# Kernel optimization log

Measured on AMD Instinct MI355X. Metric: run time of the kernel, lower is better.

Reference implementation:

```python
import jax, jax.numpy as jnp
import numpy as np
from jax import lax

C = 128; H = 28; W = 28
VID_LENS = [32, 96, 64, 48, 80, 40, 88, 64]  # sums to 512
T_TOTAL = sum(VID_LENS)


def setup_inputs() -> dict:
    key = jax.random.key(0)
    ks = jax.random.split(key, 6)
    fan2 = C * 9
    fan1 = C * 3
    return {
        "x": jax.random.normal(ks[0], (T_TOTAL, C, H, W), dtype=jnp.float32),
        "vid_lens": jnp.array(VID_LENS, dtype=jnp.int32),
        "w_sp": jax.random.normal(ks[1], (C, C, 3, 3), dtype=jnp.float32) / np.sqrt(fan2),
        "b_sp": jax.random.normal(ks[2], (C,), dtype=jnp.float32) * 0.01,
        "w_t": jax.random.normal(ks[3], (C, C, 3), dtype=jnp.float32) / np.sqrt(fan1),
        "b_t": jax.random.normal(ks[4], (C,), dtype=jnp.float32) * 0.01,
        "alpha": jnp.full((C,), 0.25, dtype=jnp.float32),  # MultiNL ~ per-channel PReLU
    }


def _forward(x, vid_lens, w_sp, b_sp, w_t, b_t, alpha):
    projection = x
    # spatial 3x3 conv, stride 1, padding 1 (SAME), NCHW
    y = lax.conv_general_dilated(
        x, w_sp, window_strides=(1, 1), padding="SAME",
        dimension_numbers=("NCHW", "OIHW", "NCHW")) + b_sp[None, :, None, None]

    # Ragged temporal conv1d (k=3, pad=1) over concatenated time axis.
    # Zero the temporal neighbors at segment boundaries so each video is
    # convolved independently (equivalent to per-segment zero padding).
    T = y.shape[0]
    ends = jnp.cumsum(vid_lens)            # segment end indices (exclusive)
    starts = ends - vid_lens               # segment start indices
    start_mask = jnp.zeros((T,), bool).at[starts].set(True)
    end_mask = jnp.zeros((T,), bool).at[ends - 1].set(True)

    y_prev = jnp.where(start_mask[:, None, None, None], 0.0, jnp.roll(y, 1, axis=0))
    y_next = jnp.where(end_mask[:, None, None, None], 0.0, jnp.roll(y, -1, axis=0))

    # conv1d along time == per-tap channel-mixing matmul
    z = (jnp.einsum("oc,tchw->tohw", w_t[:, :, 0], y_prev)
         + jnp.einsum("oc,tchw->tohw", w_t[:, :, 1], y)
         + jnp.einsum("oc,tchw->tohw", w_t[:, :, 2], y_next)
         + b_t[None, :, None, None])

    # MultiNL modeled as per-channel PReLU
    z = jnp.where(z >= 0, z, alpha[None, :, None, None] * z)
    return z + projection


def reference(x, vid_lens, w_sp, b_sp, w_t, b_t, alpha):
    out = _forward(x, vid_lens, w_sp, b_sp, w_t, b_t, alpha)
    return (out, vid_lens)  # lengths are unchanged (k=3, pad=1)
```

## Files before the change

kernel.cpp:

```cpp
#include <hip/hip_runtime.h>

#define TT   512
#define CH   128
#define HWP  784
#define NSEG 8
#define NOUT 51380224

typedef short bf16x8  __attribute__((ext_vector_type(8)));
typedef float f32x4   __attribute__((ext_vector_type(4)));
typedef int   i32x4   __attribute__((ext_vector_type(4)));
typedef unsigned short u16x4 __attribute__((ext_vector_type(4)));

__device__ inline unsigned short f2bf(float f) {
    unsigned u = __builtin_bit_cast(unsigned, f);
    u += 0x7fffu + ((u >> 16) & 1u);
    return (unsigned short)(u >> 16);
}
__device__ inline int swz(int st) { return ((st ^ (st >> 4)) & 15) << 4; }

__device__ inline void gld_lds16(const void* g, void* l) {
    __builtin_amdgcn_global_load_lds(
        (const __attribute__((address_space(1))) void*)g,
        (__attribute__((address_space(3))) void*)l, 16, 0, 0);
}

__global__ void repack_wsp(const float* __restrict__ w, short* __restrict__ wA) {
    int s = blockIdx.x * 256 + threadIdx.x;
    if (s >= 128 * 128 * 9) return;
    int co = s / 1152, r = s % 1152, ci = r / 9, kh = (r % 9) / 3, kw = r % 3;
    int tap = kh * 3 + kw;
    int dst = tap * 16384 + (co >> 4) * 2048 + (ci >> 5) * 512 +
              ((ci >> 3) & 3) * 128 + (co & 15) * 8 + (ci & 7);
    wA[dst] = (short)f2bf(w[s]);
}

__global__ void repack_wt2(const float* __restrict__ w, short* __restrict__ wAt) {
    int s = blockIdx.x * 256 + threadIdx.x;
    if (s >= 128 * 128 * 3) return;
    int o = s / 384, r = s % 384, i = r / 3, tap = r % 3;
    int dst = tap * 16384 + (o >> 4) * 2048 + (i >> 5) * 512 +
              ((i >> 3) & 3) * 128 + (o & 15) * 8 + (i & 7);
    wAt[dst] = (short)f2bf(w[s]);
}

__global__ __launch_bounds__(512, 4) void spatial_mfma(
    const float* __restrict__ x, const short* __restrict__ wA,
    const float* __restrict__ b_sp, unsigned short* __restrict__ yT)
{
    __shared__ __align__(16) short xs[282 * 128];
    const int t = blockIdx.y, blockh = blockIdx.x * 8;
    const int tid = threadIdx.x;

    for (int it = 0; it < 9; ++it) {
        int u = it * 512 + tid;
        if (u < 4480) {
            int cp = u / 70, pg = u % 70;
            int rl = pg / 7, g = pg % 7;
            int rr = blockh - 1 + rl;
            float4 f0 = make_float4(0.f, 0.f, 0.f, 0.f), f1 = f0;
            if (rr >= 0 && rr < 28) {
                const float* p0 = &x[((size_t)(t * CH + 2 * cp)) * HWP + rr * 28 + g * 4];
                f0 = *(const float4*)p0;
                f1 = *(const float4*)(p0 + HWP);
            }
            float a0[4] = {f0.x, f0.y, f0.z, f0.w}, a1[4] = {f1.x, f1.y, f1.z, f1.w};
#pragma unroll
            for (int j = 0; j < 4; ++j) {
                int st = 1 + pg * 4 + j;
                unsigned val = (unsigned)f2bf(a0[j]) | ((unsigned)f2bf(a1[j]) << 16);
                int addr = (st << 8) + (cp << 2);
                addr ^= swz(st);
                *(unsigned*)((char*)xs + addr) = val;
            }
        }
    }
    __syncthreads();

    const int wid = tid >> 6, l = tid & 63;
    const int wm = wid & 1, rg = (wid >> 1) & 1, nfh = wid >> 2;
    const int l15 = l & 15, kgrp = l >> 4;
    const int h0 = blockh + rg * 4;
    if (h0 >= 28) return;

    int st0[4], mL[4], mR[4];
#pragma unroll
    for (int nfi = 0; nfi < 4; ++nfi) {
        int pl = (nfh * 4 + nfi) * 16 + l15;
        int plc = (pl < 112) ? pl : 0;
        st0[nfi] = plc + 29 + rg * 112;
        int w28 = plc % 28;
        mL[nfi] = (w28 != 0)  ? -1 : 0;
        mR[nfi] = (w28 != 27) ? -1 : 0;
    }

    f32x4 acc[4][4];
#pragma unroll
    for (int m = 0; m < 4; ++m)
#pragma unroll
        for (int n = 0; n < 4; ++n) acc[m][n] = (f32x4){0.f, 0.f, 0.f, 0.f};

    const bf16x8* wAv = (const bf16x8*)wA;

    for (int tap = 0; tap < 9; ++tap) {
        int kh = tap / 3, kw = tap % 3;
        int off = (kh - 1) * 28 + (kw - 1);
#pragma unroll
        for (int ks = 0; ks < 4; ++ks) {
            bf16x8 a0 = wAv[((tap * 8 + wm * 4 + 0) * 4 + ks) * 64 + l];
            bf16x8 a1 = wAv[((tap * 8 + wm * 4 + 1) * 4 + ks) * 64 + l];
            bf16x8 a2 = wAv[((tap * 8 + wm * 4 + 2) * 4 + ks) * 64 + l];
            bf16x8 a3 = wAv[((tap * 8 + wm * 4 + 3) * 4 + ks) * 64 + l];
#pragma unroll
            for (int nfi = 0; nfi < 4; ++nfi) {
                int st = st0[nfi] + off;
                int addr = (st << 8) + (ks << 6) + (kgrp << 4);
                addr ^= swz(st);
                i32x4 bi = *(const i32x4*)((const char*)xs + addr);
                int msk = (kw == 0) ? mL[nfi] : ((kw == 2) ? mR[nfi] : -1);
                bi = bi & msk;
                bf16x8 b = __builtin_bit_cast(bf16x8, bi);
                acc[0][nfi] = __builtin_amdgcn_mfma_f32_16x16x32_bf16(a0, b, acc[0][nfi], 0, 0, 0);
                acc[1][nfi] = __builtin_amdgcn_mfma_f32_16x16x32_bf16(a1, b, acc[1][nfi], 0, 0, 0);
                acc[2][nfi] = __builtin_amdgcn_mfma_f32_16x16x32_bf16(a2, b, acc[2][nfi], 0, 0, 0);
                acc[3][nfi] = __builtin_amdgcn_mfma_f32_16x16x32_bf16(a3, b, acc[3][nfi], 0, 0, 0);
            }
        }
    }

#pragma unroll
    for (int m = 0; m < 4; ++m) {
        int cob = wm * 64 + m * 16 + kgrp * 4;
        float4 bs = *(const float4*)&b_sp[cob];
        float bsa[4] = {bs.x, bs.y, bs.z, bs.w};
#pragma unroll
        for (int nfi = 0; nfi < 4; ++nfi) {
            int pl = (nfh * 4 + nfi) * 16 + l15;
            if (nfh == 1 && nfi == 3) continue;
            int px = h0 * 28 + pl;
            u16x4 pk;
#pragma unroll
            for (int r = 0; r < 4; ++r) pk[r] = f2bf(acc[m][nfi][r] + bsa[r]);
            *(u16x4*)&yT[((size_t)t * HWP + px) * CH + cob] = pk;
        }
    }
}

__global__ __launch_bounds__(256, 4) void temporal_mfma(
    const unsigned short* __restrict__ yT, const short* __restrict__ wAt,
    const float* __restrict__ b_t, const float* __restrict__ alpha,
    const float* __restrict__ x, const int* __restrict__ vid_lens,
    float* __restrict__ out)
{
    __shared__ __align__(16) char ldsT[29696];

    const int chunk = blockIdx.x, t = blockIdx.y;
    const int tid = threadIdx.x, wid = tid >> 6, l = tid & 63;
    const int l15 = l & 15, kgrp = l >> 4;
    const int sx = l15 & 7;

    bool isS = false, isE = false;
    {
        int cum = 0;
        for (int s = 0; s < NSEG; ++s) {
            if (t == cum) isS = true;
            cum += vid_lens[s];
            if (t == cum - 1) isE = true;
        }
    }
    const bool tapAct[3] = {!isS, true, !isE};

    auto stage = [&](int s) {
        int tap = s >> 1, kp = s & 1;
        if (!tapAct[tap]) return;
        int tp = t + tap - 1;
        const char* yb = (const char*)yT + (size_t)tp * HWP * 256;
        char* buf = ldsT + (s & 1) * 14336;
#pragma unroll
        for (int r = 0; r < 4; ++r) {
            int c = r * 256 + wid * 64 + l;
            if (r < 3 || wid < 2) {
                int px = c >> 3, sp = c & 7;
                int ssrc = sp ^ (px & 7);
                const char* g = yb + ((size_t)(chunk * 112 + px)) * 256 + kp * 128 + ssrc * 16;
                char* ldst = buf + (r * 256 + wid * 64) * 16;
                gld_lds16(g, ldst);
            }
        }
    };

    f32x4 acc[2][7];
#pragma unroll
    for (int m = 0; m < 2; ++m)
#pragma unroll
        for (int n = 0; n < 7; ++n) acc[m][n] = (f32x4){0.f, 0.f, 0.f, 0.f};

    const bf16x8* wAv = (const bf16x8*)wAt;

    stage(0);
    __syncthreads();

    for (int s = 0; s < 6; ++s) {
        if (s < 5) stage(s + 1);
        int tap = s >> 1, kp = s & 1;
        if (tapAct[tap]) {
            const char* buf = ldsT + (s & 1) * 14336;
            bf16x8 a[2][2];
#pragma unroll
            for (int m = 0; m < 2; ++m)
#pragma unroll
                for (int k1 = 0; k1 < 2; ++k1)
                    a[m][k1] = wAv[((tap * 8 + wid * 2 + m) * 4 + kp * 2 + k1) * 64 + l];
#pragma unroll
            for (int k1 = 0; k1 < 2; ++k1) {
#pragma unroll
                for (int nf = 0; nf < 7; ++nf) {
                    int addr = (nf * 16 + l15) * 128 + ((k1 * 4 + kgrp) ^ sx) * 16;
                    i32x4 bi = *(const i32x4*)(buf + addr);
                    bf16x8 b = __builtin_bit_cast(bf16x8, bi);
                    acc[0][nf] = __builtin_amdgcn_mfma_f32_16x16x32_bf16(a[0][k1], b, acc[0][nf], 0, 0, 0);
                    acc[1][nf] = __builtin_amdgcn_mfma_f32_16x16x32_bf16(a[1][k1], b, acc[1][nf], 0, 0, 0);
                }
            }
        }
        __syncthreads();
    }

    float* fl = (float*)ldsT;
    const int wbase = wid * 1856;
#pragma unroll
    for (int m = 0; m < 2; ++m) {
#pragma unroll
        for (int nf = 0; nf < 7; ++nf)
#pragma unroll
            for (int rr = 0; rr < 4; ++rr)
                fl[wbase + (kgrp * 4 + rr) * 116 + nf * 16 + l15] = acc[m][nf][rr];
#pragma unroll
        for (int j = 0; j < 7; ++j) {
            int idx = j * 64 + l;
            int co_r = idx / 28, q = idx % 28;
            f32x4 v4 = *(const f32x4*)&fl[wbase + co_r * 116 + q * 4];
            int co_g = wid * 32 + m * 16 + co_r;
            float bt = b_t[co_g], al = alpha[co_g];
            size_t gi = ((size_t)(t * CH + co_g)) * HWP + chunk * 112 + q * 4;
            float4 xv = *(const float4*)&x[gi];
            float xr[4] = {xv.x, xv.y, xv.z, xv.w};
            float rrv[4];
#pragma unroll
            for (int e = 0; e < 4; ++e) {
                float v = v4[e] + bt;
                v = (v >= 0.f) ? v : al * v;
                rrv[e] = v + xr[e];
            }
            *(float4*)&out[gi] = make_float4(rrv[0], rrv[1], rrv[2], rrv[3]);
        }
        __syncthreads();
    }
}

__global__ void write_lens(const int* __restrict__ vid_lens, float* __restrict__ out) {
    int i = threadIdx.x;
    if (i < NSEG) out[NOUT + i] = (float)vid_lens[i];
}

extern "C" void kernel_launch(void* const* d_in, const int* in_sizes, int n_in,
                              void* d_out, int out_size, void* d_ws, size_t ws_size,
                              hipStream_t stream) {
    const float* x        = (const float*)d_in[0];
    const int*   vid_lens = (const int*)d_in[1];
    const float* w_sp     = (const float*)d_in[2];
    const float* b_sp     = (const float*)d_in[3];
    const float* w_t      = (const float*)d_in[4];
    const float* b_t      = (const float*)d_in[5];
    const float* alpha    = (const float*)d_in[6];
    float* out = (float*)d_out;

    unsigned short* yT = (unsigned short*)d_ws;
    short* wA  = (short*)((char*)d_ws + 102760448);
    short* wAt = (short*)((char*)d_ws + 102760448 + 294912);

    repack_wsp<<<576, 256, 0, stream>>>(w_sp, wA);
    repack_wt2<<<192, 256, 0, stream>>>(w_t, wAt);
    spatial_mfma<<<dim3(4, 512), 512, 0, stream>>>(x, wA, b_sp, yT);
    temporal_mfma<<<dim3(7, 512), 256, 0, stream>>>(yT, wAt, b_t, alpha, x, vid_lens, out);
    write_lens<<<1, 64, 0, stream>>>(vid_lens, out);
}
```

Measured before the change: 332.6 us.

## Pad spatial LDS tile, remap warp tiling, and write channel-interleaved 16-byte yT stores

The spatial conv LDS tile gains zero-padded border columns (30-wide rows), so the per-tap left/right edge masks go away. Each warp's tile changes from 4 channel blocks by 4 pixel fragments to 2 channel blocks by all 7 pixel fragments, which removes the wasted padded fragment. The per-tap LDS addresses are now precomputed once per tap. The output is written as 16-byte vectors in a permuted channel order, and the temporal weight repack is permuted to match. s_setprio is also added around the MFMA loops in both kernels. Risks include extra LDS, more accumulator registers, and correctness of the channel permutation.

```diff
diff --git a/kernel.cpp b/kernel.cpp
--- a/kernel.cpp
+++ b/kernel.cpp
@@ -9,14 +9,13 @@
 typedef short bf16x8  __attribute__((ext_vector_type(8)));
 typedef float f32x4   __attribute__((ext_vector_type(4)));
 typedef int   i32x4   __attribute__((ext_vector_type(4)));
-typedef unsigned short u16x4 __attribute__((ext_vector_type(4)));
+typedef unsigned short u16x8 __attribute__((ext_vector_type(8)));
 
 __device__ inline unsigned short f2bf(float f) {
     unsigned u = __builtin_bit_cast(unsigned, f);
     u += 0x7fffu + ((u >> 16) & 1u);
     return (unsigned short)(u >> 16);
 }
-__device__ inline int swz(int st) { return ((st ^ (st >> 4)) & 15) << 4; }
 
 __device__ inline void gld_lds16(const void* g, void* l) {
     __builtin_amdgcn_global_load_lds(
@@ -37,25 +36,37 @@
 __global__ void repack_wt2(const float* __restrict__ w, short* __restrict__ wAt) {
     int s = blockIdx.x * 256 + threadIdx.x;
     if (s >= 128 * 128 * 3) return;
-    int o = s / 384, r = s % 384, i = r / 3, tap = r % 3;
-    int dst = tap * 16384 + (o >> 4) * 2048 + (i >> 5) * 512 +
-              ((i >> 3) & 3) * 128 + (o & 15) * 8 + (i & 7);
-    wAt[dst] = (short)f2bf(w[s]);
+    int o = s / 384, r = s % 384, k = r / 3, tap = r % 3;
+    int ci = (k & 96) | (((k >> 2) & 1) << 4) | (((k >> 3) & 3) << 2) | (k & 3);
+    int dst = tap * 16384 + (o >> 4) * 2048 + (k >> 5) * 512 +
+              ((k >> 3) & 3) * 128 + (o & 15) * 8 + (k & 7);
+    wAt[dst] = (short)f2bf(w[o * 384 + ci * 3 + tap]);
 }
 
 __global__ __launch_bounds__(512, 4) void spatial_mfma(
     const float* __restrict__ x, const short* __restrict__ wA,
     const float* __restrict__ b_sp, unsigned short* __restrict__ yT)
 {
-    __shared__ __align__(16) short xs[282 * 128];
+    __shared__ __align__(16) short xs[300 * 128];
+    char* xsb = (char*)xs;
     const int t = blockIdx.y, blockh = blockIdx.x * 8;
     const int tid = threadIdx.x;
 
+    for (int it = 0; it < 3; ++it) {
+        int u = it * 512 + tid;
+        if (u < 1280) {
+            int cp = u & 63, rs = u >> 6;
+            int st = (rs >> 1) * 30 + (rs & 1) * 29;
+            int addr = (st << 8) | (cp << 2);
+            addr ^= ((st ^ (st >> 4)) & 15) << 4;
+            *(unsigned*)(xsb + addr) = 0u;
+        }
+    }
     for (int it = 0; it < 9; ++it) {
         int u = it * 512 + tid;
         if (u < 4480) {
-            int cp = u / 70, pg = u % 70;
-            int rl = pg / 7, g = pg % 7;
+            int cp = u & 63, pq = u >> 6;
+            int rl = pq / 7, g = pq % 7;
             int rr = blockh - 1 + rl;
             float4 f0 = make_float4(0.f, 0.f, 0.f, 0.f), f1 = f0;
             if (rr >= 0 && rr < 28) {
@@ -64,84 +75,78 @@
                 f1 = *(const float4*)(p0 + HWP);
             }
             float a0[4] = {f0.x, f0.y, f0.z, f0.w}, a1[4] = {f1.x, f1.y, f1.z, f1.w};
+            int stb = rl * 30 + g * 4 + 1;
 #pragma unroll
             for (int j = 0; j < 4; ++j) {
-                int st = 1 + pg * 4 + j;
+                int st = stb + j;
                 unsigned val = (unsigned)f2bf(a0[j]) | ((unsigned)f2bf(a1[j]) << 16);
-                int addr = (st << 8) + (cp << 2);
-                addr ^= swz(st);
-                *(unsigned*)((char*)xs + addr) = val;
+                int addr = (st << 8) | (cp << 2);
+                addr ^= ((st ^ (st >> 4)) & 15) << 4;
+                *(unsigned*)(xsb + addr) = val;
             }
         }
     }
     __syncthreads();
 
     const int wid = tid >> 6, l = tid & 63;
-    const int wm = wid & 1, rg = (wid >> 1) & 1, nfh = wid >> 2;
+    const int wm = wid & 1, rg = (wid >> 1) & 1, ms = wid >> 2;
     const int l15 = l & 15, kgrp = l >> 4;
     const int h0 = blockh + rg * 4;
     if (h0 >= 28) return;
 
-    int st0[4], mL[4], mR[4];
-#pragma unroll
-    for (int nfi = 0; nfi < 4; ++nfi) {
-        int pl = (nfh * 4 + nfi) * 16 + l15;
-        int plc = (pl < 112) ? pl : 0;
-        st0[nfi] = plc + 29 + rg * 112;
-        int w28 = plc % 28;
-        mL[nfi] = (w28 != 0)  ? -1 : 0;
-        mR[nfi] = (w28 != 27) ? -1 : 0;
-    }
-
-    f32x4 acc[4][4];
-#pragma unroll
-    for (int m = 0; m < 4; ++m)
-#pragma unroll
-        for (int n = 0; n < 4; ++n) acc[m][n] = (f32x4){0.f, 0.f, 0.f, 0.f};
+    int st0[7];
+#pragma unroll
+    for (int nf = 0; nf < 7; ++nf) {
+        int pl = nf * 16 + l15;
+        st0[nf] = (rg * 4 + pl / 28 + 1) * 30 + (pl % 28) + 1;
+    }
+
+    f32x4 acc[2][7];
+#pragma unroll
+    for (int d = 0; d < 2; ++d)
+#pragma unroll
+        for (int n = 0; n < 7; ++n) acc[d][n] = (f32x4){0.f, 0.f, 0.f, 0.f};
 
     const bf16x8* wAv = (const bf16x8*)wA;
 
     for (int tap = 0; tap < 9; ++tap) {
-        int kh = tap / 3, kw = tap % 3;
-        int off = (kh - 1) * 28 + (kw - 1);
+        int off = (tap / 3 - 1) * 30 + (tap % 3 - 1);
+        int adr[7];
+#pragma unroll
+        for (int nf = 0; nf < 7; ++nf) {
+            int st = st0[nf] + off;
+            adr[nf] = ((st << 8) | (kgrp << 4)) ^ (((st ^ (st >> 4)) & 15) << 4);
+        }
 #pragma unroll
         for (int ks = 0; ks < 4; ++ks) {
-            bf16x8 a0 = wAv[((tap * 8 + wm * 4 + 0) * 4 + ks) * 64 + l];
-            bf16x8 a1 = wAv[((tap * 8 + wm * 4 + 1) * 4 + ks) * 64 + l];
-            bf16x8 a2 = wAv[((tap * 8 + wm * 4 + 2) * 4 + ks) * 64 + l];
-            bf16x8 a3 = wAv[((tap * 8 + wm * 4 + 3) * 4 + ks) * 64 + l];
-#pragma unroll
-            for (int nfi = 0; nfi < 4; ++nfi) {
-                int st = st0[nfi] + off;
-                int addr = (st << 8) + (ks << 6) + (kgrp << 4);
-                addr ^= swz(st);
-                i32x4 bi = *(const i32x4*)((const char*)xs + addr);
-                int msk = (kw == 0) ? mL[nfi] : ((kw == 2) ? mR[nfi] : -1);
-                bi = bi & msk;
+            bf16x8 a0 = wAv[((tap * 8 + wm * 4 + ms * 2 + 0) * 4 + ks) * 64 + l];
+            bf16x8 a1 = wAv[((tap * 8 + wm * 4 + ms * 2 + 1) * 4 + ks) * 64 + l];
+            __builtin_amdgcn_s_setprio(1);
+#pragma unroll
+            for (int nf = 0; nf < 7; ++nf) {
+                i32x4 bi = *(const i32x4*)(xsb + (adr[nf] ^ (ks << 6)));
                 bf16x8 b = __builtin_bit_cast(bf16x8, bi);
-                acc[0][nfi] = __builtin_amdgcn_mfma_f32_16x16x32_bf16(a0, b, acc[0][nfi], 0, 0, 0);
-                acc[1][nfi] = __builtin_amdgcn_mfma_f32_16x16x32_bf16(a1, b, acc[1][nfi], 0, 0, 0);
-                acc[2][nfi] = __builtin_amdgcn_mfma_f32_16x16x32_bf16(a2, b, acc[2][nfi], 0, 0, 0);
-                acc[3][nfi] = __builtin_amdgcn_mfma_f32_16x16x32_bf16(a3, b, acc[3][nfi], 0, 0, 0);
-            }
-        }
-    }
-
-#pragma unroll
-    for (int m = 0; m < 4; ++m) {
-        int cob = wm * 64 + m * 16 + kgrp * 4;
-        float4 bs = *(const float4*)&b_sp[cob];
-        float bsa[4] = {bs.x, bs.y, bs.z, bs.w};
-#pragma unroll
-        for (int nfi = 0; nfi < 4; ++nfi) {
-            int pl = (nfh * 4 + nfi) * 16 + l15;
-            if (nfh == 1 && nfi == 3) continue;
-            int px = h0 * 28 + pl;
-            u16x4 pk;
-#pragma unroll
-            for (int r = 0; r < 4; ++r) pk[r] = f2bf(acc[m][nfi][r] + bsa[r]);
-            *(u16x4*)&yT[((size_t)t * HWP + px) * CH + cob] = pk;
-        }
+                acc[0][nf] = __builtin_amdgcn_mfma_f32_16x16x32_bf16(a0, b, acc[0][nf], 0, 0, 0);
+                acc[1][nf] = __builtin_amdgcn_mfma_f32_16x16x32_bf16(a1, b, acc[1][nf], 0, 0, 0);
+            }
+            __builtin_amdgcn_s_setprio(0);
+        }
+    }
+
+    float4 blo = *(const float4*)&b_sp[wm * 64 + ms * 32 + kgrp * 4];
+    float4 bhi = *(const float4*)&b_sp[wm * 64 + ms * 32 + 16 + kgrp * 4];
+    float bl[4] = {blo.x, blo.y, blo.z, blo.w}, bh[4] = {bhi.x, bhi.y, bhi.z, bhi.w};
+#pragma unroll
+    for (int nf = 0; nf < 7; ++nf) {
+        int px = h0 * 28 + nf * 16 + l15;
+        u16x8 pk;
+#pragma unroll
+        for (int r = 0; r < 4; ++r) {
+            pk[r]     = f2bf(acc[0][nf][r] + bl[r]);
+            pk[4 + r] = f2bf(acc[1][nf][r] + bh[r]);
+        }
+        char* dst = (char*)yT + ((size_t)t * HWP + px) * 256 + wm * 128 + ms * 64 + kgrp * 16;
+        *(u16x8*)dst = pk;
     }
 }
 
@@ -210,6 +215,7 @@
 #pragma unroll
                 for (int k1 = 0; k1 < 2; ++k1)
                     a[m][k1] = wAv[((tap * 8 + wid * 2 + m) * 4 + kp * 2 + k1) * 64 + l];
+            __builtin_amdgcn_s_setprio(1);
 #pragma unroll
             for (int k1 = 0; k1 < 2; ++k1) {
 #pragma unroll
@@ -221,6 +227,7 @@
                     acc[1][nf] = __builtin_amdgcn_mfma_f32_16x16x32_bf16(a[1][k1], b, acc[1][nf], 0, 0, 0);
                 }
             }
+            __builtin_amdgcn_s_setprio(0);
         }
         __syncthreads();
     }
```

Result: faster. 297.7 us (-10.5%).
